# Optimization experiments

Measured on AMD Instinct MI355X. Metric: run time of the kernel, lower is better.

Reference implementation:

```python
import jax, jax.numpy as jnp
import numpy as np

N_WIRES = 4
BATCH, SEQ, EMBED, FFN = 8, 512, 512, 2048


def setup_inputs() -> dict:
    key = jax.random.key(0)
    k_x, k_w1, k_w2 = jax.random.split(key, 3)
    x = jax.random.normal(k_x, (BATCH, SEQ, EMBED), dtype=jnp.float32)
    # Linear params (torch Linear: y = x @ W^T + b; we store pre-transposed)
    W1 = jax.random.normal(k_w1, (EMBED, FFN), dtype=jnp.float32) / np.sqrt(EMBED)
    b1 = jnp.zeros((FFN,), dtype=jnp.float32)
    W2 = jax.random.normal(k_w2, (FFN, EMBED), dtype=jnp.float32) / np.sqrt(FFN)
    b2 = jnp.zeros((EMBED,), dtype=jnp.float32)
    return {"x": x, "W1": W1, "b1": b1, "W2": W2, "b2": b2}


def reference(x, W1, b1, W2, b2):
    b, s, d = x.shape
    flat = x.reshape(b * s, d)                      # [n, d], n = b*s
    # Quantum kernel: circuit RY(x_i) then RY(-y_i) per wire on |0..0>;
    # |0..0> amplitude = prod_i cos((x_i - y_i)/2); only first n_wires feats used
    # (reset_states(1) + states.view(-1)[0] selects batch row 0 of the reshape).
    f = flat[:, :N_WIRES]                           # [n, nw]
    half_diff = (f[:, None, :] - f[None, :, :]) * 0.5   # [n, n, nw]
    gram = jnp.abs(jnp.prod(jnp.cos(half_diff), axis=-1))  # [n, n]
    out = gram @ flat                               # [n, d]
    h = jax.nn.relu(out @ W1 + b1)                  # [n, ffn]  (dropout = eval identity)
    y = h @ W2 + b2                                 # [n, d]
    return y.reshape(b, s, d)
```

## Files before the change

kernel.cpp:

```cpp
#include <hip/hip_runtime.h>
#include <hip/hip_bf16.h>
#include <stdint.h>

using bf = __bf16;
typedef __attribute__((ext_vector_type(8))) __bf16 bf16x8;
typedef __attribute__((ext_vector_type(4))) float f32x4;
typedef __attribute__((ext_vector_type(4))) int i32x4;

#define M_TOT 4096
#define D_EMB 512
#define F_FFN 2048

__device__ __forceinline__ void gload_lds16(const void* g, void* l) {
  __builtin_amdgcn_global_load_lds(
      (const __attribute__((address_space(1))) uint32_t*)g,
      (__attribute__((address_space(3))) uint32_t*)l, 16, 0, 0);
}

__device__ __forceinline__ int swz128(int row, int b) {
  return row * 128 + (b ^ ((row & 7) << 4));
}
__device__ __forceinline__ bf16x8 ldf128(const char* base, int row, int b) {
  return *(const bf16x8*)(base + swz128(row, b));
}
__device__ __forceinline__ i32x4 ldf128i(const char* base, int row, int b) {
  return *(const i32x4*)(base + swz128(row, b));
}
template <int CHUNKS>
__device__ __forceinline__ void stage_rows4(const void* gsrc, size_t ld_bytes, char* lbase,
                                            int wave, int lane) {
  const int rsub = lane >> 3, csub = lane & 7;
  const int sc = csub ^ rsub;
#pragma unroll
  for (int i = 0; i < CHUNKS / 4; ++i) {
    int chunk = wave + i * 4;
    int row = chunk * 8 + rsub;
    gload_lds16((const char*)gsrc + (size_t)row * ld_bytes + sc * 16, lbase + chunk * 1024);
  }
}
__device__ __forceinline__ int quant_i8(float x, float s) {
  float v = x * s;
  v = fminf(127.f, fmaxf(-127.f, v));
  return (int)rintf(v);
}

#define NB_SGEN 1024
#define NT_FT   2048
#define NT_W1   1024
#define NT_W2   1024

__global__ __launch_bounds__(256) void k_prep(const float* __restrict__ x,
                                              const float* __restrict__ W1,
                                              const float* __restrict__ W2,
                                              int8_t* __restrict__ fi8, bf* __restrict__ w1T,
                                              bf* __restrict__ w2T, int8_t* __restrict__ S) {
  __shared__ __align__(16) char smem[32768];
  const int bid = blockIdx.x, tid = threadIdx.x;

  if (bid < NB_SGEN) {
    char* phiL = smem;
    char* st = smem + 16384;
    const int m0 = (bid & 31) * 128;
    const int j0 = (bid >> 5) * 128;
    {
      int g = (tid < 128) ? (m0 + tid) : (j0 + tid - 128);
      float c[4], s[4];
#pragma unroll
      for (int k = 0; k < 4; ++k) {
        float f = x[(size_t)g * D_EMB + k] * 0.5f;
        sincosf(f, &s[k], &c[k]);
      }
      bf* row = (bf*)(phiL + tid * 64);
#pragma unroll
      for (int m = 0; m < 16; ++m) {
        float p = 1.0f;
#pragma unroll
        for (int k = 0; k < 4; ++k) p *= ((m >> k) & 1) ? s[k] : c[k];
        row[m] = (bf)p;
      }
#pragma unroll
      for (int m = 16; m < 32; ++m) row[m] = (bf)0.0f;
    }
    __syncthreads();

    const int wave = tid >> 6, lane = tid & 63;
    const int lr = lane & 15, lg = lane >> 4;
    const bf16x8 a0 = *(const bf16x8*)(phiL + (wave * 32 + lr) * 64 + lg * 16);
    const bf16x8 a1 = *(const bf16x8*)(phiL + (wave * 32 + 16 + lr) * 64 + lg * 16);

    const int mb0 = wave * 32 + lg * 4;
    const int key = (lr & 7) << 4;
#pragma unroll
    for (int jf = 0; jf < 8; ++jf) {
      bf16x8 b = *(const bf16x8*)(phiL + (128 + jf * 16 + lr) * 64 + lg * 16);
      f32x4 s0 = __builtin_amdgcn_mfma_f32_16x16x32_bf16(a0, b, f32x4{0.f, 0.f, 0.f, 0.f}, 0, 0, 0);
      f32x4 s1 = __builtin_amdgcn_mfma_f32_16x16x32_bf16(a1, b, f32x4{0.f, 0.f, 0.f, 0.f}, 0, 0, 0);
      uint32_t w0 = 0, w1 = 0;
#pragma unroll
      for (int r = 0; r < 4; ++r) {
        uint32_t q0 = (uint32_t)min(127, (int)rintf(fabsf(s0[r]) * 127.f));
        uint32_t q1 = (uint32_t)min(127, (int)rintf(fabsf(s1[r]) * 127.f));
        w0 |= q0 << (8 * r);
        w1 |= q1 << (8 * r);
      }
      int jrow = jf * 16 + lr;
      *(uint32_t*)(st + jrow * 128 + (mb0 ^ key)) = w0;
      *(uint32_t*)(st + jrow * 128 + ((mb0 + 16) ^ key)) = w1;
    }
    __syncthreads();
#pragma unroll
    for (int i = 0; i < 4; ++i) {
      int idx = tid + i * 256;
      int jrow = idx >> 3, seg = idx & 7;
      i32x4 v = *(const i32x4*)(st + jrow * 128 + ((seg * 16) ^ ((jrow & 7) << 4)));
      *(i32x4*)(S + (size_t)(j0 + jrow) * M_TOT + m0 + seg * 16) = v;
    }
    return;
  }

  float(*tile)[33] = (float(*)[33])smem;
  const int tx = tid & 31, ty = tid >> 5;
  if (bid < NB_SGEN + NT_FT) {
    int b2 = bid - NB_SGEN;
    int c0 = (b2 % (D_EMB / 32)) * 32, r0 = (b2 / (D_EMB / 32)) * 32;
#pragma unroll
    for (int i = 0; i < 32; i += 8)
      tile[ty + i][tx] = x[(size_t)(r0 + ty + i) * D_EMB + c0 + tx];
    __syncthreads();
#pragma unroll
    for (int i = 0; i < 32; i += 8)
      fi8[(size_t)(c0 + ty + i) * M_TOT + r0 + tx] = (int8_t)quant_i8(tile[tx][ty + i], 15.875f);
  } else if (bid < NB_SGEN + NT_FT + NT_W1) {
    int b2 = bid - NB_SGEN - NT_FT;
    int c0 = (b2 % (F_FFN / 32)) * 32, r0 = (b2 / (F_FFN / 32)) * 32;
#pragma unroll
    for (int i = 0; i < 32; i += 8)
      tile[ty + i][tx] = W1[(size_t)(r0 + ty + i) * F_FFN + c0 + tx];
    __syncthreads();
#pragma unroll
    for (int i = 0; i < 32; i += 8)
      w1T[(size_t)(c0 + ty + i) * D_EMB + r0 + tx] = (bf)tile[tx][ty + i];
  } else {
    int b2 = bid - NB_SGEN - NT_FT - NT_W1;
    int c0 = (b2 % (D_EMB / 32)) * 32, r0 = (b2 / (D_EMB / 32)) * 32;
#pragma unroll
    for (int i = 0; i < 32; i += 8)
      tile[ty + i][tx] = W2[(size_t)(r0 + ty + i) * D_EMB + c0 + tx];
    __syncthreads();
#pragma unroll
    for (int i = 0; i < 32; i += 8)
      w2T[(size_t)(c0 + ty + i) * F_FFN + r0 + tx] = (bf)tile[tx][ty + i];
  }
}

template <int OUTMODE>
__global__ __launch_bounds__(256, 3) void k_g64(const bf* __restrict__ A, const bf* __restrict__ BT,
                                                const float* __restrict__ bias, void* __restrict__ out,
                                                int N, int K) {
  constexpr int BUF = 16384;
  __shared__ __align__(16) char sm[3 * BUF];

  const int tid = threadIdx.x;
  const int wave = tid >> 6, lane = tid & 63;
  const int lr = lane & 15, lg = lane >> 4;
  const int wm = wave & 1, wn = wave >> 1;

  const int lin = blockIdx.x;
  const int e = lin & 7, jj = lin >> 3;
  const int bm = e * 8 + (jj & 7), bn = jj >> 3;
  const int m0 = bm * 64, n0 = bn * 64;

  f32x4 acc[2][2];
#pragma unroll
  for (int i = 0; i < 2; ++i)
#pragma unroll
    for (int f = 0; f < 2; ++f) acc[i][f] = f32x4{0.f, 0.f, 0.f, 0.f};

  const size_t ldb = (size_t)K * 2;
  stage_rows4<8>(A + (size_t)m0 * K, ldb, sm, wave, lane);
  stage_rows4<8>(BT + (size_t)n0 * K, ldb, sm + 8192, wave, lane);
  stage_rows4<8>(A + (size_t)m0 * K + 64, ldb, sm + BUF, wave, lane);
  stage_rows4<8>(BT + (size_t)n0 * K + 64, ldb, sm + BUF + 8192, wave, lane);

  const int NT = K / 64;
  for (int t = 0; t < NT; ++t) {
    char* aTc = sm + (t % 3) * BUF;
    char* bTc = aTc + 8192;
    if (t + 1 < NT) asm volatile("s_waitcnt vmcnt(4)" ::: "memory");
    else            asm volatile("s_waitcnt vmcnt(0)" ::: "memory");
    __builtin_amdgcn_s_barrier();

    if (t + 2 < NT) {
      char* aTn = sm + ((t + 2) % 3) * BUF;
      stage_rows4<8>(A + (size_t)m0 * K + (t + 2) * 64, ldb, aTn, wave, lane);
      stage_rows4<8>(BT + (size_t)n0 * K + (t + 2) * 64, ldb, aTn + 8192, wave, lane);
    }
#pragma unroll
    for (int ksl = 0; ksl < 2; ++ksl) {
      bf16x8 a[2], b[2];
#pragma unroll
      for (int i = 0; i < 2; ++i) a[i] = ldf128(aTc, wm * 32 + i * 16 + lr, (ksl * 32 + lg * 8) * 2);
#pragma unroll
      for (int f = 0; f < 2; ++f) b[f] = ldf128(bTc, wn * 32 + f * 16 + lr, (ksl * 32 + lg * 8) * 2);
#pragma unroll
      for (int i = 0; i < 2; ++i)
#pragma unroll
        for (int f = 0; f < 2; ++f)
          acc[i][f] = __builtin_amdgcn_mfma_f32_16x16x32_bf16(a[i], b[f], acc[i][f], 0, 0, 0);
    }
  }

#pragma unroll
  for (int f = 0; f < 2; ++f) {
    int n = n0 + wn * 32 + f * 16 + lr;
    float bv = bias[n];
#pragma unroll
    for (int i = 0; i < 2; ++i)
#pragma unroll
      for (int r = 0; r < 4; ++r) {
        int m = m0 + wm * 32 + i * 16 + lg * 4 + r;
        float v = acc[i][f][r] + bv;
        if (OUTMODE == 1) {
          v = v > 0.f ? v : 0.f;
          ((bf*)out)[(size_t)m * N + n] = (bf)v;
        } else {
          ((float*)out)[(size_t)m * N + n] = v;
        }
      }
  }
}

__global__ __launch_bounds__(256, 3) void k_gi64(const int8_t* __restrict__ S,
                                                 const int8_t* __restrict__ FT,
                                                 bf* __restrict__ outb) {
  constexpr int BUF = 16384;
  __shared__ __align__(16) char sm[3 * BUF];

  const int tid = threadIdx.x;
  const int wave = tid >> 6, lane = tid & 63;
  const int lr = lane & 15, lg = lane >> 4;
  const int wm = wave & 1, wn = wave >> 1;

  const int lin = blockIdx.x;
  const int e = lin & 7, jj = lin >> 3;
  const int bm = e * 8 + (jj & 7), bn = jj >> 3;
  const int m0 = bm * 64, n0 = bn * 64;

  i32x4 acc[2][2];
#pragma unroll
  for (int i = 0; i < 2; ++i)
#pragma unroll
    for (int f = 0; f < 2; ++f) acc[i][f] = i32x4{0, 0, 0, 0};

  stage_rows4<8>(S + (size_t)m0 * M_TOT, M_TOT, sm, wave, lane);
  stage_rows4<8>(FT + (size_t)n0 * M_TOT, M_TOT, sm + 8192, wave, lane);
  stage_rows4<8>(S + (size_t)m0 * M_TOT + 128, M_TOT, sm + BUF, wave, lane);
  stage_rows4<8>(FT + (size_t)n0 * M_TOT + 128, M_TOT, sm + BUF + 8192, wave, lane);

  constexpr int NT = M_TOT / 128;
  for (int t = 0; t < NT; ++t) {
    char* aTc = sm + (t % 3) * BUF;
    char* bTc = aTc + 8192;
    if (t + 1 < NT) asm volatile("s_waitcnt vmcnt(4)" ::: "memory");
    else            asm volatile("s_waitcnt vmcnt(0)" ::: "memory");
    __builtin_amdgcn_s_barrier();

    if (t + 2 < NT) {
      char* aTn = sm + ((t + 2) % 3) * BUF;
      stage_rows4<8>(S + (size_t)m0 * M_TOT + (t + 2) * 128, M_TOT, aTn, wave, lane);
      stage_rows4<8>(FT + (size_t)n0 * M_TOT + (t + 2) * 128, M_TOT, aTn + 8192, wave, lane);
    }
#pragma unroll
    for (int ksub = 0; ksub < 2; ++ksub) {
      i32x4 a[2], b[2];
#pragma unroll
      for (int i = 0; i < 2; ++i) a[i] = ldf128i(aTc, wm * 32 + i * 16 + lr, ksub * 64 + lg * 16);
#pragma unroll
      for (int f = 0; f < 2; ++f) b[f] = ldf128i(bTc, wn * 32 + f * 16 + lr, ksub * 64 + lg * 16);
#pragma unroll
      for (int i = 0; i < 2; ++i)
#pragma unroll
        for (int f = 0; f < 2; ++f)
          acc[i][f] = __builtin_amdgcn_mfma_i32_16x16x64_i8(a[i], b[f], acc[i][f], 0, 0, 0);
    }
  }

  constexpr float SCALE = 8.0f / 16129.0f;
#pragma unroll
  for (int f = 0; f < 2; ++f) {
    int n = n0 + wn * 32 + f * 16 + lr;
#pragma unroll
    for (int i = 0; i < 2; ++i)
#pragma unroll
      for (int r = 0; r < 4; ++r) {
        int m = m0 + wm * 32 + i * 16 + lg * 4 + r;
        outb[(size_t)m * D_EMB + n] = (bf)((float)acc[i][f][r] * SCALE);
      }
  }
}

constexpr size_t OFF_FI8  = 0;
constexpr size_t OFF_OUTB = OFF_FI8 + (size_t)D_EMB * M_TOT;
constexpr size_t OFF_W1T  = OFF_OUTB + (size_t)M_TOT * D_EMB * 2;
constexpr size_t OFF_W2T  = OFF_W1T + (size_t)F_FFN * D_EMB * 2;
constexpr size_t OFF_S    = OFF_W2T + (size_t)D_EMB * F_FFN * 2;
constexpr size_t OFF_HB   = OFF_S;

extern "C" void kernel_launch(void* const* d_in, const int* in_sizes, int n_in,
                              void* d_out, int out_size, void* d_ws, size_t ws_size,
                              hipStream_t stream) {
  const float* x  = (const float*)d_in[0];
  const float* W1 = (const float*)d_in[1];
  const float* b1 = (const float*)d_in[2];
  const float* W2 = (const float*)d_in[3];
  const float* b2 = (const float*)d_in[4];
  float* y = (float*)d_out;
  char* ws = (char*)d_ws;

  int8_t* fi8 = (int8_t*)(ws + OFF_FI8);
  bf* outb    = (bf*)(ws + OFF_OUTB);
  bf* w1T     = (bf*)(ws + OFF_W1T);
  bf* w2T     = (bf*)(ws + OFF_W2T);
  int8_t* S   = (int8_t*)(ws + OFF_S);
  bf* hb      = (bf*)(ws + OFF_HB);

  k_prep<<<dim3(NB_SGEN + NT_FT + NT_W1 + NT_W2), 256, 0, stream>>>(x, W1, W2, fi8, w1T, w2T, S);

  k_gi64<<<dim3(512), 256, 0, stream>>>(S, fi8, outb);

  k_g64<1><<<dim3(2048), 256, 0, stream>>>(outb, w1T, b1, (void*)hb, F_FFN, D_EMB);
  k_g64<0><<<dim3(512), 256, 0, stream>>>(hb, w2T, b2, (void*)y, D_EMB, F_FFN);
}
```

Baseline: 68.36 us.

## Fuse four kernel launches into one cooperative persistent kernel with grid syncs

Merges the prep, int8 gram GEMM and two bf16 FFN GEMMs into a single cooperative kernel that loops over virtual block ids and uses grid-wide syncs between phases. It falls back to separate launches if the cooperative launch fails. The aim is to remove inter-kernel launch gaps and tail effects. In exchange it adds grid-sync overhead and per-phase __syncthreads, limits the grid to at most 768 resident blocks, and runs the prep phase with the larger 48KB shared-memory footprint, which may reduce occupancy and overlap.

```diff
diff --git a/kernel.cpp b/kernel.cpp
--- a/kernel.cpp
+++ b/kernel.cpp
@@ -1,6 +1,9 @@
 #include <hip/hip_runtime.h>
 #include <hip/hip_bf16.h>
+#include <hip/hip_cooperative_groups.h>
 #include <stdint.h>
+
+namespace cg = cooperative_groups;
 
 using bf = __bf16;
 typedef __attribute__((ext_vector_type(8))) __bf16 bf16x8;
@@ -48,15 +51,14 @@
 #define NT_FT   2048
 #define NT_W1   1024
 #define NT_W2   1024
-
-__global__ __launch_bounds__(256) void k_prep(const float* __restrict__ x,
-                                              const float* __restrict__ W1,
-                                              const float* __restrict__ W2,
-                                              int8_t* __restrict__ fi8, bf* __restrict__ w1T,
-                                              bf* __restrict__ w2T, int8_t* __restrict__ S) {
-  __shared__ __align__(16) char smem[32768];
-  const int bid = blockIdx.x, tid = threadIdx.x;
-
+#define NPREP   (NB_SGEN + NT_FT + NT_W1 + NT_W2)
+
+__device__ __forceinline__ void phase_prep(const float* __restrict__ x,
+                                           const float* __restrict__ W1,
+                                           const float* __restrict__ W2,
+                                           int8_t* __restrict__ fi8, bf* __restrict__ w1T,
+                                           bf* __restrict__ w2T, int8_t* __restrict__ S,
+                                           int bid, int tid, char* smem) {
   if (bid < NB_SGEN) {
     char* phiL = smem;
     char* st = smem + 16384;
@@ -115,6 +117,7 @@
       i32x4 v = *(const i32x4*)(st + jrow * 128 + ((seg * 16) ^ ((jrow & 7) << 4)));
       *(i32x4*)(S + (size_t)(j0 + jrow) * M_TOT + m0 + seg * 16) = v;
     }
+    __syncthreads();
     return;
   }
 
@@ -151,21 +154,84 @@
     for (int i = 0; i < 32; i += 8)
       w2T[(size_t)(c0 + ty + i) * F_FFN + r0 + tx] = (bf)tile[tx][ty + i];
   }
-}
-
-template <int OUTMODE>
-__global__ __launch_bounds__(256, 3) void k_g64(const bf* __restrict__ A, const bf* __restrict__ BT,
-                                                const float* __restrict__ bias, void* __restrict__ out,
-                                                int N, int K) {
+  __syncthreads();
+}
+
+__device__ __forceinline__ void phase_gi64(const int8_t* __restrict__ S,
+                                           const int8_t* __restrict__ FT,
+                                           bf* __restrict__ outb, int lin, int tid, char* sm) {
   constexpr int BUF = 16384;
-  __shared__ __align__(16) char sm[3 * BUF];
-
-  const int tid = threadIdx.x;
   const int wave = tid >> 6, lane = tid & 63;
   const int lr = lane & 15, lg = lane >> 4;
   const int wm = wave & 1, wn = wave >> 1;
 
-  const int lin = blockIdx.x;
+  const int e = lin & 7, jj = lin >> 3;
+  const int bm = e * 8 + (jj & 7), bn = jj >> 3;
+  const int m0 = bm * 64, n0 = bn * 64;
+
+  i32x4 acc[2][2];
+#pragma unroll
+  for (int i = 0; i < 2; ++i)
+#pragma unroll
+    for (int f = 0; f < 2; ++f) acc[i][f] = i32x4{0, 0, 0, 0};
+
+  stage_rows4<8>(S + (size_t)m0 * M_TOT, M_TOT, sm, wave, lane);
+  stage_rows4<8>(FT + (size_t)n0 * M_TOT, M_TOT, sm + 8192, wave, lane);
+  stage_rows4<8>(S + (size_t)m0 * M_TOT + 128, M_TOT, sm + BUF, wave, lane);
+  stage_rows4<8>(FT + (size_t)n0 * M_TOT + 128, M_TOT, sm + BUF + 8192, wave, lane);
+
+  constexpr int NT = M_TOT / 128;
+  for (int t = 0; t < NT; ++t) {
+    char* aTc = sm + (t % 3) * BUF;
+    char* bTc = aTc + 8192;
+    if (t + 1 < NT) asm volatile("s_waitcnt vmcnt(4)" ::: "memory");
+    else            asm volatile("s_waitcnt vmcnt(0)" ::: "memory");
+    __builtin_amdgcn_s_barrier();
+
+    if (t + 2 < NT) {
+      char* aTn = sm + ((t + 2) % 3) * BUF;
+      stage_rows4<8>(S + (size_t)m0 * M_TOT + (t + 2) * 128, M_TOT, aTn, wave, lane);
+      stage_rows4<8>(FT + (size_t)n0 * M_TOT + (t + 2) * 128, M_TOT, aTn + 8192, wave, lane);
+    }
+#pragma unroll
+    for (int ksub = 0; ksub < 2; ++ksub) {
+      i32x4 a[2], b[2];
+#pragma unroll
+      for (int i = 0; i < 2; ++i) a[i] = ldf128i(aTc, wm * 32 + i * 16 + lr, ksub * 64 + lg * 16);
+#pragma unroll
+      for (int f = 0; f < 2; ++f) b[f] = ldf128i(bTc, wn * 32 + f * 16 + lr, ksub * 64 + lg * 16);
+#pragma unroll
+      for (int i = 0; i < 2; ++i)
+#pragma unroll
+        for (int f = 0; f < 2; ++f)
+          acc[i][f] = __builtin_amdgcn_mfma_i32_16x16x64_i8(a[i], b[f], acc[i][f], 0, 0, 0);
+    }
+  }
+  __syncthreads();
+
+  constexpr float SCALE = 8.0f / 16129.0f;
+#pragma unroll
+  for (int f = 0; f < 2; ++f) {
+    int n = n0 + wn * 32 + f * 16 + lr;
+#pragma unroll
+    for (int i = 0; i < 2; ++i)
+#pragma unroll
+      for (int r = 0; r < 4; ++r) {
+        int m = m0 + wm * 32 + i * 16 + lg * 4 + r;
+        outb[(size_t)m * D_EMB + n] = (bf)((float)acc[i][f][r] * SCALE);
+      }
+  }
+}
+
+template <int OUTMODE>
+__device__ __forceinline__ void phase_g64(const bf* __restrict__ A, const bf* __restrict__ BT,
+                                          const float* __restrict__ bias, void* __restrict__ out,
+                                          int N, int K, int lin, int tid, char* sm) {
+  constexpr int BUF = 16384;
+  const int wave = tid >> 6, lane = tid & 63;
+  const int lr = lane & 15, lg = lane >> 4;
+  const int wm = wave & 1, wn = wave >> 1;
+
   const int e = lin & 7, jj = lin >> 3;
   const int bm = e * 8 + (jj & 7), bn = jj >> 3;
   const int m0 = bm * 64, n0 = bn * 64;
@@ -209,6 +275,7 @@
           acc[i][f] = __builtin_amdgcn_mfma_f32_16x16x32_bf16(a[i], b[f], acc[i][f], 0, 0, 0);
     }
   }
+  __syncthreads();
 
 #pragma unroll
   for (int f = 0; f < 2; ++f) {
@@ -230,73 +297,42 @@
   }
 }
 
-__global__ __launch_bounds__(256, 3) void k_gi64(const int8_t* __restrict__ S,
-                                                 const int8_t* __restrict__ FT,
-                                                 bf* __restrict__ outb) {
-  constexpr int BUF = 16384;
-  __shared__ __align__(16) char sm[3 * BUF];
-
+__global__ __launch_bounds__(256, 3) void k_mega(const float* x, const float* W1, const float* W2,
+                                                 const float* b1, const float* b2,
+                                                 int8_t* fi8, bf* w1T, bf* w2T, int8_t* S,
+                                                 bf* outb, bf* hb, float* y) {
+  __shared__ __align__(16) char smem[49152];
+  cg::grid_group grid = cg::this_grid();
   const int tid = threadIdx.x;
-  const int wave = tid >> 6, lane = tid & 63;
-  const int lr = lane & 15, lg = lane >> 4;
-  const int wm = wave & 1, wn = wave >> 1;
-
-  const int lin = blockIdx.x;
-  const int e = lin & 7, jj = lin >> 3;
-  const int bm = e * 8 + (jj & 7), bn = jj >> 3;
-  const int m0 = bm * 64, n0 = bn * 64;
-
-  i32x4 acc[2][2];
-#pragma unroll
-  for (int i = 0; i < 2; ++i)
-#pragma unroll
-    for (int f = 0; f < 2; ++f) acc[i][f] = i32x4{0, 0, 0, 0};
-
-  stage_rows4<8>(S + (size_t)m0 * M_TOT, M_TOT, sm, wave, lane);
-  stage_rows4<8>(FT + (size_t)n0 * M_TOT, M_TOT, sm + 8192, wave, lane);
-  stage_rows4<8>(S + (size_t)m0 * M_TOT + 128, M_TOT, sm + BUF, wave, lane);
-  stage_rows4<8>(FT + (size_t)n0 * M_TOT + 128, M_TOT, sm + BUF + 8192, wave, lane);
-
-  constexpr int NT = M_TOT / 128;
-  for (int t = 0; t < NT; ++t) {
-    char* aTc = sm + (t % 3) * BUF;
-    char* bTc = aTc + 8192;
-    if (t + 1 < NT) asm volatile("s_waitcnt vmcnt(4)" ::: "memory");
-    else            asm volatile("s_waitcnt vmcnt(0)" ::: "memory");
-    __builtin_amdgcn_s_barrier();
-
-    if (t + 2 < NT) {
-      char* aTn = sm + ((t + 2) % 3) * BUF;
-      stage_rows4<8>(S + (size_t)m0 * M_TOT + (t + 2) * 128, M_TOT, aTn, wave, lane);
-      stage_rows4<8>(FT + (size_t)n0 * M_TOT + (t + 2) * 128, M_TOT, aTn + 8192, wave, lane);
-    }
-#pragma unroll
-    for (int ksub = 0; ksub < 2; ++ksub) {
-      i32x4 a[2], b[2];
-#pragma unroll
-      for (int i = 0; i < 2; ++i) a[i] = ldf128i(aTc, wm * 32 + i * 16 + lr, ksub * 64 + lg * 16);
-#pragma unroll
-      for (int f = 0; f < 2; ++f) b[f] = ldf128i(bTc, wn * 32 + f * 16 + lr, ksub * 64 + lg * 16);
-#pragma unroll
-      for (int i = 0; i < 2; ++i)
-#pragma unroll
-        for (int f = 0; f < 2; ++f)
-          acc[i][f] = __builtin_amdgcn_mfma_i32_16x16x64_i8(a[i], b[f], acc[i][f], 0, 0, 0);
-    }
-  }
-
-  constexpr float SCALE = 8.0f / 16129.0f;
-#pragma unroll
-  for (int f = 0; f < 2; ++f) {
-    int n = n0 + wn * 32 + f * 16 + lr;
-#pragma unroll
-    for (int i = 0; i < 2; ++i)
-#pragma unroll
-      for (int r = 0; r < 4; ++r) {
-        int m = m0 + wm * 32 + i * 16 + lg * 4 + r;
-        outb[(size_t)m * D_EMB + n] = (bf)((float)acc[i][f][r] * SCALE);
-      }
-  }
+  const int stride = (int)gridDim.x;
+
+  for (int v = blockIdx.x; v < NPREP; v += stride)
+    phase_prep(x, W1, W2, fi8, w1T, w2T, S, v, tid, smem);
+  grid.sync();
+  for (int v = blockIdx.x; v < 512; v += stride)
+    phase_gi64(S, fi8, outb, v, tid, smem);
+  grid.sync();
+  for (int v = blockIdx.x; v < 2048; v += stride)
+    phase_g64<1>(outb, w1T, b1, (void*)hb, F_FFN, D_EMB, v, tid, smem);
+  grid.sync();
+  for (int v = blockIdx.x; v < 512; v += stride)
+    phase_g64<0>(hb, w2T, b2, (void*)y, D_EMB, F_FFN, v, tid, smem);
+}
+
+__global__ __launch_bounds__(256) void k_prep_sep(const float* x, const float* W1, const float* W2,
+                                                  int8_t* fi8, bf* w1T, bf* w2T, int8_t* S) {
+  __shared__ __align__(16) char smem[32768];
+  phase_prep(x, W1, W2, fi8, w1T, w2T, S, blockIdx.x, threadIdx.x, smem);
+}
+__global__ __launch_bounds__(256, 3) void k_gi64_sep(const int8_t* S, const int8_t* FT, bf* outb) {
+  __shared__ __align__(16) char smem[49152];
+  phase_gi64(S, FT, outb, blockIdx.x, threadIdx.x, smem);
+}
+template <int OUTMODE>
+__global__ __launch_bounds__(256, 3) void k_g64_sep(const bf* A, const bf* BT, const float* bias,
+                                                    void* out, int N, int K) {
+  __shared__ __align__(16) char smem[49152];
+  phase_g64<OUTMODE>(A, BT, bias, out, N, K, blockIdx.x, threadIdx.x, smem);
 }
 
 constexpr size_t OFF_FI8  = 0;
@@ -324,10 +360,25 @@
   int8_t* S   = (int8_t*)(ws + OFF_S);
   bf* hb      = (bf*)(ws + OFF_HB);
 
-  k_prep<<<dim3(NB_SGEN + NT_FT + NT_W1 + NT_W2), 256, 0, stream>>>(x, W1, W2, fi8, w1T, w2T, S);
-
-  k_gi64<<<dim3(512), 256, 0, stream>>>(S, fi8, outb);
-
-  k_g64<1><<<dim3(2048), 256, 0, stream>>>(outb, w1T, b1, (void*)hb, F_FFN, D_EMB);
-  k_g64<0><<<dim3(512), 256, 0, stream>>>(hb, w2T, b2, (void*)y, D_EMB, F_FFN);
-}
+  int maxb = 0;
+  hipError_t oe = hipOccupancyMaxActiveBlocksPerMultiprocessor(&maxb, k_mega, 256, 0);
+  bool coop_ok = false;
+  if (oe == hipSuccess && maxb >= 1) {
+    int grid = 256 * maxb;
+    if (grid > 768) grid = 768;
+    const float* xa = x; const float* w1a = W1; const float* w2a = W2;
+    const float* b1a = b1; const float* b2a = b2;
+    int8_t* fia = fi8; bf* w1ta = w1T; bf* w2ta = w2T; int8_t* Sa = S;
+    bf* outa = outb; bf* hba = hb; float* ya = y;
+    void* args[] = {&xa, &w1a, &w2a, &b1a, &b2a, &fia, &w1ta, &w2ta, &Sa, &outa, &hba, &ya};
+    hipError_t le = hipLaunchCooperativeKernel((const void*)k_mega, dim3(grid), dim3(256),
+                                               args, 0, stream);
+    coop_ok = (le == hipSuccess);
+  }
+  if (!coop_ok) {
+    k_prep_sep<<<dim3(NPREP), 256, 0, stream>>>(x, W1, W2, fi8, w1T, w2T, S);
+    k_gi64_sep<<<dim3(512), 256, 0, stream>>>(S, fi8, outb);
+    k_g64_sep<1><<<dim3(2048), 256, 0, stream>>>(outb, w1T, b1, (void*)hb, F_FFN, D_EMB);
+    k_g64_sep<0><<<dim3(512), 256, 0, stream>>>(hb, w2T, b2, (void*)y, D_EMB, F_FFN);
+  }
+}
```

Measured after the change: 266.7 us. 290% more time.
